# Optimization experiments

Measured on AMD Instinct MI355X. Metric: run time of the kernel, lower is better.

The kernel has to match this reference:

```python
import jax, jax.numpy as jnp
import numpy as np

B, T, H = 32, 4096, 512


def setup_inputs() -> dict:
    key = jax.random.key(0)
    k1, k2, k3, k4, k5 = jax.random.split(key, 5)
    stdv = 1.0 / np.sqrt(2 * H)
    stdv_v = 1.0 / np.sqrt(H)
    return {
        "hidden": jax.random.normal(k1, (B, H), dtype=jnp.float32),
        "encoder_outputs": jax.random.normal(k2, (T, B, H), dtype=jnp.float32),
        "W_attn": jax.random.uniform(k3, (H, 2 * H), minval=-stdv, maxval=stdv, dtype=jnp.float32),
        "b_attn": jax.random.uniform(k4, (H,), minval=-stdv, maxval=stdv, dtype=jnp.float32),
        "v": jax.random.uniform(k5, (H,), minval=-stdv_v, maxval=stdv_v, dtype=jnp.float32),
    }


def reference(hidden, encoder_outputs, W_attn, b_attn, v):
    # hidden: [B, H]; encoder_outputs: [T, B, H]
    T_ = encoder_outputs.shape[0]
    h = jnp.broadcast_to(hidden[None, :, :], (T_,) + hidden.shape).transpose(1, 0, 2)  # [B,T,H]
    enc = encoder_outputs.transpose(1, 0, 2)  # [B,T,H]
    cat = jnp.concatenate([h, enc], axis=2)  # [B,T,2H]
    # Linear(2H -> H) then legacy F.softmax with implicit dim=0 for 3D input (batch axis)
    energy = jax.nn.softmax(jnp.einsum('btk,hk->bth', cat, W_attn) + b_attn, axis=0)  # [B,T,H]
    # bmm(v[B,1,H], energy^T[B,H,T]) -> [B,1,T] -> squeeze -> [B,T]
    scores = jnp.einsum('h,bth->bt', v, energy)
    return jax.nn.relu(scores)[:, None, :]  # [B,1,T]
```

## Files before the change

kernel.cpp:

```cpp
#include <hip/hip_runtime.h>
#include <hip/hip_bf16.h>

#define B_ 32
#define T_ 4096
#define H_ 512
#define TILE_T 2
#define M_TILE 64
#define BK 64
#define KSTEPS 8
#define NTHREADS 256

typedef __attribute__((ext_vector_type(8))) short short8;
typedef __attribute__((ext_vector_type(8))) __bf16 bf16x8;
typedef __attribute__((ext_vector_type(4))) float f32x4;

__device__ __forceinline__ short f2bf(float f) {
    unsigned u = __builtin_bit_cast(unsigned, f);
    u = (u + 0x7fffu + ((u >> 16) & 1u)) >> 16;
    return (short)u;
}

__device__ __forceinline__ short8 pack8(f32x4 a, f32x4 b) {
    union { unsigned u[4]; short8 s; } r;
    asm("v_cvt_pk_bf16_f32 %0, %1, %2" : "=v"(r.u[0]) : "v"(a[0]), "v"(a[1]));
    asm("v_cvt_pk_bf16_f32 %0, %1, %2" : "=v"(r.u[1]) : "v"(a[2]), "v"(a[3]));
    asm("v_cvt_pk_bf16_f32 %0, %1, %2" : "=v"(r.u[2]) : "v"(b[0]), "v"(b[1]));
    asm("v_cvt_pk_bf16_f32 %0, %1, %2" : "=v"(r.u[3]) : "v"(b[2]), "v"(b[3]));
    return r.s;
}

__global__ void prep_w2f(const float* __restrict__ W, short* __restrict__ w2f) {
    int idx = blockIdx.x * 256 + threadIdx.x;
    int j    = idx & 7;
    int lane = (idx >> 3) & 63;
    int ni   = (idx >> 9) & 3;
    int ck   = (idx >> 11) & 15;
    int c    = (idx >> 15) & 7;
    int h = c * 64 + ni * 16 + (lane & 15);
    int k = ck * 32 + (lane >> 4) * 8 + j;
    w2f[idx] = f2bf(W[h * (2 * H_) + H_ + k]);
}

__global__ void prep_hid(const float* __restrict__ hidden,
                         const float* __restrict__ W,
                         const float* __restrict__ bias,
                         float* __restrict__ hidproj) {
    __shared__ float hrow[H_];
    int b = blockIdx.y;
    int h = blockIdx.x * 128 + threadIdx.x;
    for (int i = threadIdx.x; i < H_; i += 128) hrow[i] = hidden[b * H_ + i];
    __syncthreads();
    const float* wr = W + (size_t)h * (2 * H_);
    float acc = bias[h];
#pragma unroll 4
    for (int k = 0; k < H_; k += 4) {
        acc += hrow[k]     * wr[k];
        acc += hrow[k + 1] * wr[k + 1];
        acc += hrow[k + 2] * wr[k + 2];
        acc += hrow[k + 3] * wr[k + 3];
    }
    hidproj[b * H_ + h] = acc;
}

__global__ void finish(const float* __restrict__ sp, float* __restrict__ out) {
    int i = blockIdx.x * 256 + threadIdx.x;
    out[i] = fmaxf(sp[i] + sp[131072 + i], 0.f);
}

__global__ __launch_bounds__(NTHREADS, 3)
void attn_main(const float* __restrict__ enc,
               const float* __restrict__ hidproj,
               const short* __restrict__ w2f,
               const float* __restrict__ vvec,
               float* __restrict__ spart)
{
    __shared__ __align__(16) short lds_a[2][M_TILE * BK];

    const int tid  = threadIdx.x;
    const int lane = tid & 63;
    const int wid  = tid >> 6;
    const int bid  = blockIdx.x;
    const int tau  = ((bid >> 4) << 3) | (bid & 7);
    const int eta  = (bid >> 3) & 1;
    const int t0   = tau * TILE_T;
    const int lo   = lane & 15;
    const int hi4  = lane >> 4;
    const int cblk = eta * 4 + wid;

    f32x4 acc[4][4];
#pragma unroll
    for (int i = 0; i < 4; ++i)
#pragma unroll
        for (int j = 0; j < 4; ++j) acc[i][j] = f32x4{0.f, 0.f, 0.f, 0.f};

    const short* wbase = w2f + (size_t)cblk * 32768 + lane * 8;

    const int arow = tid >> 2;
    const int akc  = tid & 3;
    const float* abase = enc + (size_t)(t0 * B_ + arow) * H_ + akc * 16;
    const int aw0 = arow * BK + (((2 * akc)     ^ (arow & 7)) << 3);
    const int aw1 = arow * BK + (((2 * akc + 1) ^ (arow & 7)) << 3);

    {
        f32x4 y0 = *(const f32x4*)(abase);     f32x4 y1 = *(const f32x4*)(abase + 4);
        f32x4 y2 = *(const f32x4*)(abase + 8); f32x4 y3 = *(const f32x4*)(abase + 12);
        *(short8*)&lds_a[0][aw0] = pack8(y0, y1);
        *(short8*)&lds_a[0][aw1] = pack8(y2, y3);
        asm volatile("s_waitcnt lgkmcnt(0)" ::: "memory");
        __builtin_amdgcn_s_barrier();
    }

#define KSUB(S, BQ)                                                               \
    {                                                                             \
        bf16x8 af[4];                                                             \
        _Pragma("unroll")                                                         \
        for (int mi = 0; mi < 4; ++mi) {                                          \
            int r = mi * 16 + lo;                                                 \
            af[mi] = *(const bf16x8*)&ab[r * BK + ((((S) * 4 + hi4) ^ (r & 7)) << 3)]; \
        }                                                                         \
        __builtin_amdgcn_s_setprio(1);                                            \
        _Pragma("unroll")                                                         \
        for (int mi = 0; mi < 4; ++mi)                                            \
            _Pragma("unroll")                                                     \
            for (int ni = 0; ni < 4; ++ni)                                        \
                acc[mi][ni] = __builtin_amdgcn_mfma_f32_16x16x32_bf16(            \
                    af[mi], BQ[ni], acc[mi][ni], 0, 0, 0);                        \
        __builtin_amdgcn_s_setprio(0);                                            \
    }

#pragma unroll 1
    for (int kk = 0; kk < KSTEPS; ++kk) {
        const int cur = kk & 1;
        const bool pf = (kk + 1) < KSTEPS;
        const short* __restrict__ ab = &lds_a[cur][0];
        short* __restrict__ adst = &lds_a[cur ^ 1][0];

        bf16x8 b0[4], b1[4];
#pragma unroll
        for (int ni = 0; ni < 4; ++ni) b0[ni] = *(const bf16x8*)(wbase + ((kk * 2 + 0) * 4 + ni) * 512);
#pragma unroll
        for (int ni = 0; ni < 4; ++ni) b1[ni] = *(const bf16x8*)(wbase + ((kk * 2 + 1) * 4 + ni) * 512);

        f32x4 x0, x1, x2, x3;
        if (pf) {
            const float* asrc = abase + (size_t)(kk + 1) * BK;
            x0 = *(const f32x4*)(asrc);      x1 = *(const f32x4*)(asrc + 4);
            x2 = *(const f32x4*)(asrc + 8);  x3 = *(const f32x4*)(asrc + 12);
        }

        KSUB(0, b0)
        if (pf) *(short8*)&adst[aw0] = pack8(x0, x1);
        KSUB(1, b1)
        if (pf) *(short8*)&adst[aw1] = pack8(x2, x3);

        asm volatile("s_waitcnt lgkmcnt(0)" ::: "memory");
        __builtin_amdgcn_s_barrier();
    }
#undef KSUB

    {
        float hp[2][4][4];
#pragma unroll
        for (int par = 0; par < 2; ++par)
#pragma unroll
            for (int j = 0; j < 4; ++j) {
                int b = par * 16 + hi4 * 4 + j;
#pragma unroll
                for (int ni = 0; ni < 4; ++ni)
                    hp[par][j][ni] = hidproj[b * H_ + cblk * 64 + ni * 16 + lo];
            }
#pragma unroll
        for (int mi = 0; mi < 4; ++mi)
#pragma unroll
            for (int ni = 0; ni < 4; ++ni)
#pragma unroll
                for (int j = 0; j < 4; ++j)
                    acc[mi][ni][j] += hp[mi & 1][j][ni];
    }

    float vh[4];
#pragma unroll
    for (int ni = 0; ni < 4; ++ni) vh[ni] = vvec[cblk * 64 + ni * 16 + lo];

    float scp[4][4];
#pragma unroll
    for (int tl2 = 0; tl2 < 2; ++tl2) {
        const int m0 = tl2 * 2, m1 = tl2 * 2 + 1;
#pragma unroll
        for (int ni = 0; ni < 4; ++ni) {
            float mx = -1e30f;
#pragma unroll
            for (int j = 0; j < 4; ++j) {
                mx = fmaxf(mx, acc[m0][ni][j]);
                mx = fmaxf(mx, acc[m1][ni][j]);
            }
            mx = fmaxf(mx, __shfl_xor(mx, 16));
            mx = fmaxf(mx, __shfl_xor(mx, 32));
            float e0[4], e1[4];
            float sum = 0.f;
#pragma unroll
            for (int j = 0; j < 4; ++j) {
                e0[j] = __expf(acc[m0][ni][j] - mx);
                e1[j] = __expf(acc[m1][ni][j] - mx);
                sum += e0[j] + e1[j];
            }
            sum += __shfl_xor(sum, 16);
            sum += __shfl_xor(sum, 32);
            float rs = vh[ni] / sum;
#pragma unroll
            for (int j = 0; j < 4; ++j) {
                if (ni == 0) { scp[m0][j] = e0[j] * rs; scp[m1][j] = e1[j] * rs; }
                else         { scp[m0][j] += e0[j] * rs; scp[m1][j] += e1[j] * rs; }
            }
        }
    }

#pragma unroll
    for (int mi = 0; mi < 4; ++mi)
#pragma unroll
        for (int j = 0; j < 4; ++j) {
            float x = scp[mi][j];
            x += __shfl_xor(x, 1);
            x += __shfl_xor(x, 2);
            x += __shfl_xor(x, 4);
            x += __shfl_xor(x, 8);
            scp[mi][j] = x;
        }

    __syncthreads();
    float* red = (float*)&lds_a[0][0];
    if (lo == 0) {
#pragma unroll
        for (int mi = 0; mi < 4; ++mi)
#pragma unroll
            for (int j = 0; j < 4; ++j)
                red[wid * 64 + mi * 16 + hi4 * 4 + j] = scp[mi][j];
    }
    __syncthreads();
    if (tid < M_TILE) {
        float s = red[tid] + red[64 + tid] + red[128 + tid] + red[192 + tid];
        int b   = tid & 31;
        int tl2 = tid >> 5;
        spart[(size_t)eta * 131072 + (size_t)b * T_ + (t0 + tl2)] = s;
    }
}

extern "C" void kernel_launch(void* const* d_in, const int* in_sizes, int n_in,
                              void* d_out, int out_size, void* d_ws, size_t ws_size,
                              hipStream_t stream) {
    const float* hidden = (const float*)d_in[0];
    const float* enc    = (const float*)d_in[1];
    const float* W      = (const float*)d_in[2];
    const float* bias   = (const float*)d_in[3];
    const float* v      = (const float*)d_in[4];
    float* out = (float*)d_out;

    float* hidproj = (float*)d_ws;
    short* w2f     = (short*)((char*)d_ws + 65536);
    float* spart   = (float*)((char*)d_ws + 65536 + 524288);

    prep_w2f<<<1024, 256, 0, stream>>>(W, w2f);
    prep_hid<<<dim3(4, 32), 128, 0, stream>>>(hidden, W, bias, hidproj);
    attn_main<<<4096, NTHREADS, 0, stream>>>(enc, hidproj, w2f, v, spart);
    finish<<<512, 256, 0, stream>>>(spart, out);
}
```

Before: 121.2 us.

## Load full K tile into LDS once, cover all H columns per block, drop finish kernel

Each block now uses 8 waves covering all 512 output columns, so the encoder tile is read and converted to bf16 only once instead of twice across two column-half blocks. The whole 64x512 A tile is staged into a single 64KB LDS buffer upfront, which removes the per-k-step barriers and double buffering. Only the W fragments are software-pipelined from global memory. The final reduction applies ReLU and writes the output directly, which removes the partial-sum buffer and the separate finish kernel. The cost is a large LDS footprint and a bulk load phase that does not overlap with the MFMA work, and this may limit occupancy.

Result: faster. 116.0 us (-4.3%).

```diff
diff --git a/kernel.cpp b/kernel.cpp
--- a/kernel.cpp
+++ b/kernel.cpp
@@ -4,12 +4,10 @@
 #define B_ 32
 #define T_ 4096
 #define H_ 512
-#define TILE_T 2
 #define M_TILE 64
-#define BK 64
-#define KSTEPS 8
-#define NTHREADS 256
-
+#define NTHREADS 512
+
+typedef __attribute__((ext_vector_type(4))) short short4v;
 typedef __attribute__((ext_vector_type(8))) short short8;
 typedef __attribute__((ext_vector_type(8))) __bf16 bf16x8;
 typedef __attribute__((ext_vector_type(4))) float f32x4;
@@ -20,12 +18,10 @@
     return (short)u;
 }
 
-__device__ __forceinline__ short8 pack8(f32x4 a, f32x4 b) {
-    union { unsigned u[4]; short8 s; } r;
+__device__ __forceinline__ short4v pack4(f32x4 a) {
+    union { unsigned u[2]; short4v s; } r;
     asm("v_cvt_pk_bf16_f32 %0, %1, %2" : "=v"(r.u[0]) : "v"(a[0]), "v"(a[1]));
     asm("v_cvt_pk_bf16_f32 %0, %1, %2" : "=v"(r.u[1]) : "v"(a[2]), "v"(a[3]));
-    asm("v_cvt_pk_bf16_f32 %0, %1, %2" : "=v"(r.u[2]) : "v"(b[0]), "v"(b[1]));
-    asm("v_cvt_pk_bf16_f32 %0, %1, %2" : "=v"(r.u[3]) : "v"(b[2]), "v"(b[3]));
     return r.s;
 }
 
@@ -62,30 +58,53 @@
     hidproj[b * H_ + h] = acc;
 }
 
-__global__ void finish(const float* __restrict__ sp, float* __restrict__ out) {
-    int i = blockIdx.x * 256 + threadIdx.x;
-    out[i] = fmaxf(sp[i] + sp[131072 + i], 0.f);
-}
-
-__global__ __launch_bounds__(NTHREADS, 3)
+__global__ __launch_bounds__(NTHREADS, 4)
 void attn_main(const float* __restrict__ enc,
                const float* __restrict__ hidproj,
                const short* __restrict__ w2f,
                const float* __restrict__ vvec,
-               float* __restrict__ spart)
+               float* __restrict__ out)
 {
-    __shared__ __align__(16) short lds_a[2][M_TILE * BK];
+    __shared__ __align__(16) short lds_a[M_TILE * H_];
 
     const int tid  = threadIdx.x;
     const int lane = tid & 63;
     const int wid  = tid >> 6;
-    const int bid  = blockIdx.x;
-    const int tau  = ((bid >> 4) << 3) | (bid & 7);
-    const int eta  = (bid >> 3) & 1;
-    const int t0   = tau * TILE_T;
     const int lo   = lane & 15;
     const int hi4  = lane >> 4;
-    const int cblk = eta * 4 + wid;
+    const int t0   = blockIdx.x * 2;
+
+    {
+        const float* sp = enc + (size_t)blockIdx.x * (M_TILE * H_) + tid * 4;
+        const int th    = tid >> 7;
+        const int half  = (tid & 1) * 8;
+        const int cb    = (tid & 127) >> 1;
+        char* lb = (char*)lds_a;
+#define ST(I, X) { short4v p = pack4(X); \
+        *(short4v*)(lb + ((I)*4 + th) * 1024 + ((cb ^ (((I)*4 + th) & 7)) * 16) + half) = p; }
+        f32x4 x0  = *(const f32x4*)(sp +  0 * 2048);
+        f32x4 x1  = *(const f32x4*)(sp +  1 * 2048);
+        f32x4 x2  = *(const f32x4*)(sp +  2 * 2048);
+        f32x4 x3  = *(const f32x4*)(sp +  3 * 2048);
+        f32x4 x4  = *(const f32x4*)(sp +  4 * 2048);
+        f32x4 x5  = *(const f32x4*)(sp +  5 * 2048);
+        f32x4 x6  = *(const f32x4*)(sp +  6 * 2048);
+        f32x4 x7  = *(const f32x4*)(sp +  7 * 2048);
+        ST(0, x0) ST(1, x1) ST(2, x2) ST(3, x3)
+        f32x4 x8  = *(const f32x4*)(sp +  8 * 2048);
+        f32x4 x9  = *(const f32x4*)(sp +  9 * 2048);
+        f32x4 x10 = *(const f32x4*)(sp + 10 * 2048);
+        f32x4 x11 = *(const f32x4*)(sp + 11 * 2048);
+        ST(4, x4) ST(5, x5) ST(6, x6) ST(7, x7)
+        f32x4 x12 = *(const f32x4*)(sp + 12 * 2048);
+        f32x4 x13 = *(const f32x4*)(sp + 13 * 2048);
+        f32x4 x14 = *(const f32x4*)(sp + 14 * 2048);
+        f32x4 x15 = *(const f32x4*)(sp + 15 * 2048);
+        ST(8, x8) ST(9, x9) ST(10, x10) ST(11, x11)
+        ST(12, x12) ST(13, x13) ST(14, x14) ST(15, x15)
+#undef ST
+    }
+    __syncthreads();
 
     f32x4 acc[4][4];
 #pragma unroll
@@ -93,30 +112,16 @@
 #pragma unroll
         for (int j = 0; j < 4; ++j) acc[i][j] = f32x4{0.f, 0.f, 0.f, 0.f};
 
-    const short* wbase = w2f + (size_t)cblk * 32768 + lane * 8;
-
-    const int arow = tid >> 2;
-    const int akc  = tid & 3;
-    const float* abase = enc + (size_t)(t0 * B_ + arow) * H_ + akc * 16;
-    const int aw0 = arow * BK + (((2 * akc)     ^ (arow & 7)) << 3);
-    const int aw1 = arow * BK + (((2 * akc + 1) ^ (arow & 7)) << 3);
-
-    {
-        f32x4 y0 = *(const f32x4*)(abase);     f32x4 y1 = *(const f32x4*)(abase + 4);
-        f32x4 y2 = *(const f32x4*)(abase + 8); f32x4 y3 = *(const f32x4*)(abase + 12);
-        *(short8*)&lds_a[0][aw0] = pack8(y0, y1);
-        *(short8*)&lds_a[0][aw1] = pack8(y2, y3);
-        asm volatile("s_waitcnt lgkmcnt(0)" ::: "memory");
-        __builtin_amdgcn_s_barrier();
-    }
-
-#define KSUB(S, BQ)                                                               \
+    const short* wbase = w2f + (size_t)wid * 32768 + lane * 8;
+    const int xm = lo & 7;
+
+#define KSUB(S4, BQ)                                                              \
     {                                                                             \
         bf16x8 af[4];                                                             \
         _Pragma("unroll")                                                         \
         for (int mi = 0; mi < 4; ++mi) {                                          \
             int r = mi * 16 + lo;                                                 \
-            af[mi] = *(const bf16x8*)&ab[r * BK + ((((S) * 4 + hi4) ^ (r & 7)) << 3)]; \
+            af[mi] = *(const bf16x8*)&lds_a[r * 512 + (((S4) + hi4) ^ xm) * 8];   \
         }                                                                         \
         __builtin_amdgcn_s_setprio(1);                                            \
         _Pragma("unroll")                                                         \
@@ -128,33 +133,23 @@
         __builtin_amdgcn_s_setprio(0);                                            \
     }
 
+    bf16x8 bqA[4], bqB[4];
+#pragma unroll
+    for (int ni = 0; ni < 4; ++ni) bqA[ni] = *(const bf16x8*)(wbase + (0 * 4 + ni) * 512);
+
 #pragma unroll 1
-    for (int kk = 0; kk < KSTEPS; ++kk) {
-        const int cur = kk & 1;
-        const bool pf = (kk + 1) < KSTEPS;
-        const short* __restrict__ ab = &lds_a[cur][0];
-        short* __restrict__ adst = &lds_a[cur ^ 1][0];
-
-        bf16x8 b0[4], b1[4];
-#pragma unroll
-        for (int ni = 0; ni < 4; ++ni) b0[ni] = *(const bf16x8*)(wbase + ((kk * 2 + 0) * 4 + ni) * 512);
-#pragma unroll
-        for (int ni = 0; ni < 4; ++ni) b1[ni] = *(const bf16x8*)(wbase + ((kk * 2 + 1) * 4 + ni) * 512);
-
-        f32x4 x0, x1, x2, x3;
-        if (pf) {
-            const float* asrc = abase + (size_t)(kk + 1) * BK;
-            x0 = *(const f32x4*)(asrc);      x1 = *(const f32x4*)(asrc + 4);
-            x2 = *(const f32x4*)(asrc + 8);  x3 = *(const f32x4*)(asrc + 12);
+    for (int kk = 0; kk < 8; ++kk) {
+        const int s0 = kk * 2;
+#pragma unroll
+        for (int ni = 0; ni < 4; ++ni)
+            bqB[ni] = *(const bf16x8*)(wbase + ((s0 + 1) * 4 + ni) * 512);
+        KSUB(s0 * 4, bqA)
+        if (kk < 7) {
+#pragma unroll
+            for (int ni = 0; ni < 4; ++ni)
+                bqA[ni] = *(const bf16x8*)(wbase + ((s0 + 2) * 4 + ni) * 512);
         }
-
-        KSUB(0, b0)
-        if (pf) *(short8*)&adst[aw0] = pack8(x0, x1);
-        KSUB(1, b1)
-        if (pf) *(short8*)&adst[aw1] = pack8(x2, x3);
-
-        asm volatile("s_waitcnt lgkmcnt(0)" ::: "memory");
-        __builtin_amdgcn_s_barrier();
+        KSUB((s0 + 1) * 4, bqB)
     }
 #undef KSUB
 
@@ -167,7 +162,7 @@
                 int b = par * 16 + hi4 * 4 + j;
 #pragma unroll
                 for (int ni = 0; ni < 4; ++ni)
-                    hp[par][j][ni] = hidproj[b * H_ + cblk * 64 + ni * 16 + lo];
+                    hp[par][j][ni] = hidproj[b * H_ + wid * 64 + ni * 16 + lo];
             }
 #pragma unroll
         for (int mi = 0; mi < 4; ++mi)
@@ -180,7 +175,7 @@
 
     float vh[4];
 #pragma unroll
-    for (int ni = 0; ni < 4; ++ni) vh[ni] = vvec[cblk * 64 + ni * 16 + lo];
+    for (int ni = 0; ni < 4; ++ni) vh[ni] = vvec[wid * 64 + ni * 16 + lo];
 
     float scp[4][4];
 #pragma unroll
@@ -228,7 +223,7 @@
         }
 
     __syncthreads();
-    float* red = (float*)&lds_a[0][0];
+    float* red = (float*)&lds_a[0];
     if (lo == 0) {
 #pragma unroll
         for (int mi = 0; mi < 4; ++mi)
@@ -238,10 +233,12 @@
     }
     __syncthreads();
     if (tid < M_TILE) {
-        float s = red[tid] + red[64 + tid] + red[128 + tid] + red[192 + tid];
+        float s = 0.f;
+#pragma unroll
+        for (int w = 0; w < 8; ++w) s += red[w * 64 + tid];
         int b   = tid & 31;
         int tl2 = tid >> 5;
-        spart[(size_t)eta * 131072 + (size_t)b * T_ + (t0 + tl2)] = s;
+        out[(size_t)b * T_ + (t0 + tl2)] = fmaxf(s, 0.f);
     }
 }
 
@@ -257,10 +254,8 @@
 
     float* hidproj = (float*)d_ws;
     short* w2f     = (short*)((char*)d_ws + 65536);
-    float* spart   = (float*)((char*)d_ws + 65536 + 524288);
 
     prep_w2f<<<1024, 256, 0, stream>>>(W, w2f);
     prep_hid<<<dim3(4, 32), 128, 0, stream>>>(hidden, W, bias, hidproj);
-    attn_main<<<4096, NTHREADS, 0, stream>>>(enc, hidproj, w2f, v, spart);
-    finish<<<512, 256, 0, stream>>>(spart, out);
-}
+    attn_main<<<T_ * B_ / (M_TILE), NTHREADS, 0, stream>>>(enc, hidproj, w2f, v, out);
+}
```

## Shrink tile to one timestep, load full K slab into LDS upfront, 8 waves

Applied to the files above, without the earlier changes.

Each block now handles one timestep (32 batch rows) and one half of H, with 512 threads split across output columns. The whole 32x512 activation slab is converted to bf16 and staged in LDS in a single up-front pass instead of a double-buffered K loop, and W fragments are register double-buffered. The aim is to remove per-K-step barriers and give more parallelism and occupancy. In exchange each block streams the full W half with less reuse per row and has no overlap between the activation load and the MFMA work.

Result: slower. 144.8 us (+19.4%).

```diff
diff --git a/kernel.cpp b/kernel.cpp
--- a/kernel.cpp
+++ b/kernel.cpp
@@ -4,13 +4,10 @@
 #define B_ 32
 #define T_ 4096
 #define H_ 512
-#define TILE_T 2
-#define M_TILE 64
-#define BK 64
-#define KSTEPS 8
-#define NTHREADS 256
-
-typedef __attribute__((ext_vector_type(8))) short short8;
+#define M_TILE 32
+#define NTHREADS 512
+
+typedef __attribute__((ext_vector_type(4))) short short4v;
 typedef __attribute__((ext_vector_type(8))) __bf16 bf16x8;
 typedef __attribute__((ext_vector_type(4))) float f32x4;
 
@@ -20,12 +17,10 @@
     return (short)u;
 }
 
-__device__ __forceinline__ short8 pack8(f32x4 a, f32x4 b) {
-    union { unsigned u[4]; short8 s; } r;
+__device__ __forceinline__ short4v pack4(f32x4 a) {
+    union { unsigned u[2]; short4v s; } r;
     asm("v_cvt_pk_bf16_f32 %0, %1, %2" : "=v"(r.u[0]) : "v"(a[0]), "v"(a[1]));
     asm("v_cvt_pk_bf16_f32 %0, %1, %2" : "=v"(r.u[1]) : "v"(a[2]), "v"(a[3]));
-    asm("v_cvt_pk_bf16_f32 %0, %1, %2" : "=v"(r.u[2]) : "v"(b[0]), "v"(b[1]));
-    asm("v_cvt_pk_bf16_f32 %0, %1, %2" : "=v"(r.u[3]) : "v"(b[2]), "v"(b[3]));
     return r.s;
 }
 
@@ -67,156 +62,143 @@
     out[i] = fmaxf(sp[i] + sp[131072 + i], 0.f);
 }
 
-__global__ __launch_bounds__(NTHREADS, 3)
+__global__ __launch_bounds__(NTHREADS, 4)
 void attn_main(const float* __restrict__ enc,
                const float* __restrict__ hidproj,
                const short* __restrict__ w2f,
                const float* __restrict__ vvec,
                float* __restrict__ spart)
 {
-    __shared__ __align__(16) short lds_a[2][M_TILE * BK];
+    __shared__ __align__(16) short lds_a[M_TILE * H_];
+    __shared__ float red[8 * M_TILE];
 
     const int tid  = threadIdx.x;
     const int lane = tid & 63;
     const int wid  = tid >> 6;
+    const int lo   = lane & 15;
+    const int hi4  = lane >> 4;
+    const int xm   = lo & 7;
     const int bid  = blockIdx.x;
     const int tau  = ((bid >> 4) << 3) | (bid & 7);
     const int eta  = (bid >> 3) & 1;
-    const int t0   = tau * TILE_T;
-    const int lo   = lane & 15;
-    const int hi4  = lane >> 4;
-    const int cblk = eta * 4 + wid;
-
-    f32x4 acc[4][4];
-#pragma unroll
-    for (int i = 0; i < 4; ++i)
-#pragma unroll
-        for (int j = 0; j < 4; ++j) acc[i][j] = f32x4{0.f, 0.f, 0.f, 0.f};
-
+
+    const int cblk = eta * 4 + (wid >> 1);
+    const int nib  = (wid & 1) * 2;
     const short* wbase = w2f + (size_t)cblk * 32768 + lane * 8;
 
-    const int arow = tid >> 2;
-    const int akc  = tid & 3;
-    const float* abase = enc + (size_t)(t0 * B_ + arow) * H_ + akc * 16;
-    const int aw0 = arow * BK + (((2 * akc)     ^ (arow & 7)) << 3);
-    const int aw1 = arow * BK + (((2 * akc + 1) ^ (arow & 7)) << 3);
-
     {
-        f32x4 y0 = *(const f32x4*)(abase);     f32x4 y1 = *(const f32x4*)(abase + 4);
-        f32x4 y2 = *(const f32x4*)(abase + 8); f32x4 y3 = *(const f32x4*)(abase + 12);
-        *(short8*)&lds_a[0][aw0] = pack8(y0, y1);
-        *(short8*)&lds_a[0][aw1] = pack8(y2, y3);
-        asm volatile("s_waitcnt lgkmcnt(0)" ::: "memory");
-        __builtin_amdgcn_s_barrier();
-    }
+        const float* ap = enc + (size_t)tau * (M_TILE * H_) + tid * 4;
+        const int rbase = tid >> 7;
+        const int cb    = (tid & 127) >> 1;
+        const int hb    = (tid & 1) * 8;
+        char* lb = (char*)lds_a;
+#define STW(I, X) { int r_ = (I) * 4 + rbase;                                     \
+        *(short4v*)(lb + r_ * 1024 + (((cb) ^ (r_ & 7)) << 4) + hb) = pack4(X); }
+        f32x4 x0, x1, x2, x3;
+        x0 = *(const f32x4*)(ap + 0 * 2048);
+        x1 = *(const f32x4*)(ap + 1 * 2048);
+        x2 = *(const f32x4*)(ap + 2 * 2048);
+        x3 = *(const f32x4*)(ap + 3 * 2048);
+        STW(0, x0) STW(1, x1) STW(2, x2) STW(3, x3)
+        x0 = *(const f32x4*)(ap + 4 * 2048);
+        x1 = *(const f32x4*)(ap + 5 * 2048);
+        x2 = *(const f32x4*)(ap + 6 * 2048);
+        x3 = *(const f32x4*)(ap + 7 * 2048);
+        STW(4, x0) STW(5, x1) STW(6, x2) STW(7, x3)
+#undef STW
+    }
+    asm volatile("s_waitcnt lgkmcnt(0)" ::: "memory");
+    __builtin_amdgcn_s_barrier();
+
+    f32x4 acc[2][2];
+#pragma unroll
+    for (int i = 0; i < 2; ++i)
+#pragma unroll
+        for (int j = 0; j < 2; ++j) acc[i][j] = f32x4{0.f, 0.f, 0.f, 0.f};
+
+#define BLD(DST, CK)                                                              \
+    { _Pragma("unroll")                                                           \
+      for (int ni_ = 0; ni_ < 2; ++ni_)                                           \
+          DST[ni_] = *(const bf16x8*)(wbase + (((CK) * 4) + nib + ni_) * 512); }
 
 #define KSUB(S, BQ)                                                               \
     {                                                                             \
-        bf16x8 af[4];                                                             \
+        bf16x8 af_[2];                                                            \
         _Pragma("unroll")                                                         \
-        for (int mi = 0; mi < 4; ++mi) {                                          \
-            int r = mi * 16 + lo;                                                 \
-            af[mi] = *(const bf16x8*)&ab[r * BK + ((((S) * 4 + hi4) ^ (r & 7)) << 3)]; \
+        for (int mi = 0; mi < 2; ++mi) {                                          \
+            int r_ = mi * 16 + lo;                                                \
+            af_[mi] = *(const bf16x8*)((char*)lds_a + r_ * 1024 +                 \
+                                       (((((S) * 4) + hi4) ^ xm) << 4));          \
         }                                                                         \
         __builtin_amdgcn_s_setprio(1);                                            \
         _Pragma("unroll")                                                         \
-        for (int mi = 0; mi < 4; ++mi)                                            \
+        for (int mi = 0; mi < 2; ++mi)                                            \
             _Pragma("unroll")                                                     \
-            for (int ni = 0; ni < 4; ++ni)                                        \
+            for (int ni = 0; ni < 2; ++ni)                                        \
                 acc[mi][ni] = __builtin_amdgcn_mfma_f32_16x16x32_bf16(            \
-                    af[mi], BQ[ni], acc[mi][ni], 0, 0, 0);                        \
+                    af_[mi], BQ[ni], acc[mi][ni], 0, 0, 0);                       \
         __builtin_amdgcn_s_setprio(0);                                            \
     }
 
-#pragma unroll 1
-    for (int kk = 0; kk < KSTEPS; ++kk) {
-        const int cur = kk & 1;
-        const bool pf = (kk + 1) < KSTEPS;
-        const short* __restrict__ ab = &lds_a[cur][0];
-        short* __restrict__ adst = &lds_a[cur ^ 1][0];
-
-        bf16x8 b0[4], b1[4];
-#pragma unroll
-        for (int ni = 0; ni < 4; ++ni) b0[ni] = *(const bf16x8*)(wbase + ((kk * 2 + 0) * 4 + ni) * 512);
-#pragma unroll
-        for (int ni = 0; ni < 4; ++ni) b1[ni] = *(const bf16x8*)(wbase + ((kk * 2 + 1) * 4 + ni) * 512);
-
-        f32x4 x0, x1, x2, x3;
-        if (pf) {
-            const float* asrc = abase + (size_t)(kk + 1) * BK;
-            x0 = *(const f32x4*)(asrc);      x1 = *(const f32x4*)(asrc + 4);
-            x2 = *(const f32x4*)(asrc + 8);  x3 = *(const f32x4*)(asrc + 12);
-        }
-
-        KSUB(0, b0)
-        if (pf) *(short8*)&adst[aw0] = pack8(x0, x1);
-        KSUB(1, b1)
-        if (pf) *(short8*)&adst[aw1] = pack8(x2, x3);
-
-        asm volatile("s_waitcnt lgkmcnt(0)" ::: "memory");
-        __builtin_amdgcn_s_barrier();
-    }
+#define KPAIR(S)                                                                  \
+    BLD(bqB, (S) + 1)                                                             \
+    KSUB((S), bqA)                                                                \
+    BLD(bqA, ((S) + 2) & 15)                                                      \
+    KSUB((S) + 1, bqB)
+
+    bf16x8 bqA[2], bqB[2];
+    BLD(bqA, 0)
+    KPAIR(0) KPAIR(2) KPAIR(4) KPAIR(6)
+    KPAIR(8) KPAIR(10) KPAIR(12) KPAIR(14)
+#undef KPAIR
 #undef KSUB
+#undef BLD
 
     {
-        float hp[2][4][4];
-#pragma unroll
-        for (int par = 0; par < 2; ++par)
+#pragma unroll
+        for (int mi = 0; mi < 2; ++mi)
 #pragma unroll
             for (int j = 0; j < 4; ++j) {
-                int b = par * 16 + hi4 * 4 + j;
-#pragma unroll
-                for (int ni = 0; ni < 4; ++ni)
-                    hp[par][j][ni] = hidproj[b * H_ + cblk * 64 + ni * 16 + lo];
+                int b = mi * 16 + hi4 * 4 + j;
+#pragma unroll
+                for (int ni = 0; ni < 2; ++ni)
+                    acc[mi][ni][j] += hidproj[b * H_ + cblk * 64 + (nib + ni) * 16 + lo];
             }
-#pragma unroll
-        for (int mi = 0; mi < 4; ++mi)
-#pragma unroll
-            for (int ni = 0; ni < 4; ++ni)
-#pragma unroll
-                for (int j = 0; j < 4; ++j)
-                    acc[mi][ni][j] += hp[mi & 1][j][ni];
-    }
-
-    float vh[4];
-#pragma unroll
-    for (int ni = 0; ni < 4; ++ni) vh[ni] = vvec[cblk * 64 + ni * 16 + lo];
-
-    float scp[4][4];
-#pragma unroll
-    for (int tl2 = 0; tl2 < 2; ++tl2) {
-        const int m0 = tl2 * 2, m1 = tl2 * 2 + 1;
-#pragma unroll
-        for (int ni = 0; ni < 4; ++ni) {
-            float mx = -1e30f;
+    }
+
+    float scp[2][4];
+#pragma unroll
+    for (int ni = 0; ni < 2; ++ni) {
+        float mx = -1e30f;
+#pragma unroll
+        for (int mi = 0; mi < 2; ++mi)
+#pragma unroll
+            for (int j = 0; j < 4; ++j) mx = fmaxf(mx, acc[mi][ni][j]);
+        mx = fmaxf(mx, __shfl_xor(mx, 16));
+        mx = fmaxf(mx, __shfl_xor(mx, 32));
+        float e[2][4];
+        float sum = 0.f;
+#pragma unroll
+        for (int mi = 0; mi < 2; ++mi)
 #pragma unroll
             for (int j = 0; j < 4; ++j) {
-                mx = fmaxf(mx, acc[m0][ni][j]);
-                mx = fmaxf(mx, acc[m1][ni][j]);
+                e[mi][j] = __expf(acc[mi][ni][j] - mx);
+                sum += e[mi][j];
             }
-            mx = fmaxf(mx, __shfl_xor(mx, 16));
-            mx = fmaxf(mx, __shfl_xor(mx, 32));
-            float e0[4], e1[4];
-            float sum = 0.f;
+        sum += __shfl_xor(sum, 16);
+        sum += __shfl_xor(sum, 32);
+        float rs = vvec[cblk * 64 + (nib + ni) * 16 + lo] / sum;
+#pragma unroll
+        for (int mi = 0; mi < 2; ++mi)
 #pragma unroll
             for (int j = 0; j < 4; ++j) {
-                e0[j] = __expf(acc[m0][ni][j] - mx);
-                e1[j] = __expf(acc[m1][ni][j] - mx);
-                sum += e0[j] + e1[j];
+                if (ni == 0) scp[mi][j]  = e[mi][j] * rs;
+                else         scp[mi][j] += e[mi][j] * rs;
             }
-            sum += __shfl_xor(sum, 16);
-            sum += __shfl_xor(sum, 32);
-            float rs = vh[ni] / sum;
-#pragma unroll
-            for (int j = 0; j < 4; ++j) {
-                if (ni == 0) { scp[m0][j] = e0[j] * rs; scp[m1][j] = e1[j] * rs; }
-                else         { scp[m0][j] += e0[j] * rs; scp[m1][j] += e1[j] * rs; }
-            }
-        }
-    }
-
-#pragma unroll
-    for (int mi = 0; mi < 4; ++mi)
+    }
+
+#pragma unroll
+    for (int mi = 0; mi < 2; ++mi)
 #pragma unroll
         for (int j = 0; j < 4; ++j) {
             float x = scp[mi][j];
@@ -227,21 +209,21 @@
             scp[mi][j] = x;
         }
 
-    __syncthreads();
-    float* red = (float*)&lds_a[0][0];
     if (lo == 0) {
 #pragma unroll
-        for (int mi = 0; mi < 4; ++mi)
+        for (int mi = 0; mi < 2; ++mi)
 #pragma unroll
             for (int j = 0; j < 4; ++j)
-                red[wid * 64 + mi * 16 + hi4 * 4 + j] = scp[mi][j];
-    }
-    __syncthreads();
+                red[wid * M_TILE + mi * 16 + hi4 * 4 + j] = scp[mi][j];
+    }
+    asm volatile("s_waitcnt lgkmcnt(0)" ::: "memory");
+    __builtin_amdgcn_s_barrier();
+
     if (tid < M_TILE) {
-        float s = red[tid] + red[64 + tid] + red[128 + tid] + red[192 + tid];
-        int b   = tid & 31;
-        int tl2 = tid >> 5;
-        spart[(size_t)eta * 131072 + (size_t)b * T_ + (t0 + tl2)] = s;
+        float s = 0.f;
+#pragma unroll
+        for (int w = 0; w < 8; ++w) s += red[w * M_TILE + tid];
+        spart[(size_t)eta * 131072 + (size_t)tid * T_ + tau] = s;
     }
 }
 
@@ -261,6 +243,6 @@
 
     prep_w2f<<<1024, 256, 0, stream>>>(W, w2f);
     prep_hid<<<dim3(4, 32), 128, 0, stream>>>(hidden, W, bias, hidproj);
-    attn_main<<<4096, NTHREADS, 0, stream>>>(enc, hidproj, w2f, v, spart);
+    attn_main<<<8192, NTHREADS, 0, stream>>>(enc, hidproj, w2f, v, spart);
     finish<<<512, 256, 0, stream>>>(spart, out);
 }
```
